# Kernel optimization log

Measured on AMD Instinct MI355X. Metric: run time of the kernel, lower is better.

Reference implementation:

```python
import jax, jax.numpy as jnp
import numpy as np

N = 100000      # nodes
E = 1600000     # edges (avg degree 16)
D_IN, D_H, D_OUT = 128, 128, 64
EPS = 1e-5      # BatchNorm1d eps


def setup_inputs() -> dict:
    key = jax.random.key(0)
    ks = jax.random.split(key, 8)
    x = jax.random.normal(ks[0], (N, D_IN), jnp.float32)
    edge_index = jax.random.randint(ks[1], (2, E), 0, N, dtype=jnp.int64)

    def glorot(k, i, o):
        return jax.random.normal(k, (i, o), jnp.float32) * np.float32(1.0 / np.sqrt(i))

    return {
        "x": x,
        "edge_index": edge_index,
        "W1": glorot(ks[2], D_IN, D_H), "b1": jnp.zeros((D_H,), jnp.float32),
        "g1": jnp.ones((D_H,), jnp.float32), "be1": jnp.zeros((D_H,), jnp.float32),
        "W2": glorot(ks[3], D_H, D_H), "b2": jnp.zeros((D_H,), jnp.float32),
        "g2": jnp.ones((D_H,), jnp.float32), "be2": jnp.zeros((D_H,), jnp.float32),
        "W3": glorot(ks[4], D_H, D_OUT), "b3": jnp.zeros((D_OUT,), jnp.float32),
    }


def gcn_conv(h, W, b, src, dst, norm_e, self_norm):
    # GCNConv: D^{-1/2}(A+I)D^{-1/2} h W + b  (self-loops handled analytically)
    hw = h @ W                                  # [N, out]
    msg = hw[src] * norm_e[:, None]             # [E, out] gather + scale
    agg = jax.ops.segment_sum(msg, dst, num_segments=N)
    return agg + hw * self_norm[:, None] + b


def batchnorm(x, g, b):
    mu = jnp.mean(x, axis=0)
    var = jnp.var(x, axis=0)
    return (x - mu) * jax.lax.rsqrt(var + EPS) * g + b


def reference(x, edge_index, W1, b1, g1, be1, W2, b2, g2, be2, W3, b3):
    src, dst = edge_index[0], edge_index[1]
    # degrees including self-loop
    deg = jax.ops.segment_sum(jnp.ones((E,), jnp.float32), dst, num_segments=N) + 1.0
    dis = jax.lax.rsqrt(deg)                    # deg^{-1/2}
    norm_e = dis[src] * dis[dst]                # per-edge norm
    self_norm = dis * dis                       # self-loop norm deg^{-1}

    h = jax.nn.relu(batchnorm(gcn_conv(x, W1, b1, src, dst, norm_e, self_norm), g1, be1))
    h = jax.nn.relu(batchnorm(gcn_conv(h, W2, b2, src, dst, norm_e, self_norm), g2, be2))
    return gcn_conv(h, W3, b3, src, dst, norm_e, self_norm)
```

## Files before the change

kernel.cpp:

```cpp
#include <hip/hip_runtime.h>
#include <hip/hip_bf16.h>

#define BN_EPS 1e-5f
#define BINSH 9
#define MAXNB 200
#define NBLK 256

typedef __attribute__((ext_vector_type(8))) short bf16x8v;
typedef __attribute__((ext_vector_type(4))) float f32x4v;

__device__ __forceinline__ float u2f(unsigned x) { return __uint_as_float(x); }
__device__ __forceinline__ unsigned short f2bf(float f) {
    union { __hip_bfloat16 h; unsigned short u; } cv;
    cv.h = __float2bfloat16(f);
    return cv.u;
}

__device__ __forceinline__ int edge_at(const void* p, long long i, int is64) {
    return is64 ? (int)((const long long*)p)[i] : ((const int*)p)[i];
}

__device__ __forceinline__ int detect_is64(const void* eidx, int* sflag, int t) {
    if (t == 0) {
        const int* e32 = (const int*)eidx;
        int nz = 0;
        for (int i = 0; i < 64; ++i) nz += (e32[2 * i + 1] != 0);
        *sflag = (nz == 0) ? 1 : 0;
    }
    return 0;
}

__global__ __launch_bounds__(256) void histA_kernel(const void* __restrict__ eidx,
                                                    int* __restrict__ hist2dT,
                                                    int* __restrict__ binhist,
                                                    int E, int NB, int per_block) {
    __shared__ int lh[MAXNB];
    __shared__ int sflag;
    const int t = threadIdx.x;
    detect_is64(eidx, &sflag, t);
    for (int i = t; i < NB; i += 256) lh[i] = 0;
    __syncthreads();
    const int is64 = sflag;
    long long base = (long long)blockIdx.x * per_block;
    long long lim  = base + per_block;
    if (lim > E) lim = E;
    for (long long e = base + t; e < lim; e += 256) {
        int d = edge_at(eidx, (long long)E + e, is64);
        atomicAdd(&lh[d >> BINSH], 1);
    }
    __syncthreads();
    for (int i = t; i < NB; i += 256) {
        hist2dT[i * NBLK + blockIdx.x] = lh[i];
        atomicAdd(&binhist[i], lh[i]);
    }
}

__global__ void binscan_kernel(const int* __restrict__ binhist, int* __restrict__ binrp, int NB) {
    __shared__ int s[256];
    const int t = threadIdx.x;
    int v = (t < NB) ? binhist[t] : 0;
    s[t] = v;
    __syncthreads();
    for (int off = 1; off < 256; off <<= 1) {
        int x = (t >= off) ? s[t - off] : 0;
        __syncthreads();
        s[t] += x;
        __syncthreads();
    }
    if (t < NB) binrp[t] = s[t] - v;
    if (t == 0) binrp[NB] = s[255];
}

__global__ __launch_bounds__(256) void colscan_kernel(int* __restrict__ hist2dT,
                                                      const int* __restrict__ binrp) {
    __shared__ int s[256];
    const int b = blockIdx.x;
    const int t = threadIdx.x;
    int v = hist2dT[b * NBLK + t];
    s[t] = v;
    __syncthreads();
    for (int off = 1; off < 256; off <<= 1) {
        int x = (t >= off) ? s[t - off] : 0;
        __syncthreads();
        s[t] += x;
        __syncthreads();
    }
    hist2dT[b * NBLK + t] = binrp[b] + s[t] - v;
}

__global__ __launch_bounds__(256) void passB_kernel(const void* __restrict__ eidx,
                                                    const int* __restrict__ hist2dT,
                                                    int2* __restrict__ ibuf,
                                                    int E, int NB, int per_block) {
    __shared__ int lbase[MAXNB];
    __shared__ int lcur[MAXNB];
    __shared__ int sflag;
    const int t = threadIdx.x;
    detect_is64(eidx, &sflag, t);
    for (int i = t; i < NB; i += 256) {
        lbase[i] = hist2dT[i * NBLK + blockIdx.x];
        lcur[i]  = 0;
    }
    __syncthreads();
    const int is64 = sflag;
    long long base = (long long)blockIdx.x * per_block;
    long long lim  = base + per_block;
    if (lim > E) lim = E;
    for (long long e = base + t; e < lim; e += 256) {
        int sN = edge_at(eidx, e, is64);
        int d  = edge_at(eidx, (long long)E + e, is64);
        int b  = d >> BINSH;
        int pos = lbase[b] + atomicAdd(&lcur[b], 1);
        ibuf[pos] = make_int2(sN, d);
    }
}

__global__ __launch_bounds__(256) void binsort2_kernel(const int2* __restrict__ ibuf,
                                                       const int* __restrict__ binrp,
                                                       int* __restrict__ rp,
                                                       float* __restrict__ dis,
                                                       int2* __restrict__ ep, int N) {
    const int b  = blockIdx.x;
    const int d0 = b << BINSH;
    const int dc = min(1 << BINSH, N - d0);
    __shared__ int lcnt[1 << BINSH];
    __shared__ int lofs[1 << BINSH];
    __shared__ int s2[256];
    const int t = threadIdx.x;
    lcnt[t] = 0; lcnt[t + 256] = 0;
    __syncthreads();
    const int ib0 = binrp[b], ib1 = binrp[b + 1];
    const int nE  = ib1 - ib0;
    for (int i = t; i < nE; i += 256) {
        int2 sd = ibuf[ib0 + i];
        atomicAdd(&lcnt[sd.y - d0], 1);
    }
    __syncthreads();
    const int c0 = lcnt[2 * t], c1 = lcnt[2 * t + 1];
    const int pair = c0 + c1;
    s2[t] = pair;
    __syncthreads();
    for (int off = 1; off < 256; off <<= 1) {
        int x = (t >= off) ? s2[t - off] : 0;
        __syncthreads();
        s2[t] += x;
        __syncthreads();
    }
    const int pexcl = s2[t] - pair;
    if (2 * t < dc) {
        rp[d0 + 2 * t + 1] = ib0 + pexcl + c0;
        dis[d0 + 2 * t]    = rsqrtf((float)c0 + 1.0f);
    }
    if (2 * t + 1 < dc) {
        rp[d0 + 2 * t + 2] = ib0 + pexcl + pair;
        dis[d0 + 2 * t + 1] = rsqrtf((float)c1 + 1.0f);
    }
    if (b == 0 && t == 0) rp[0] = 0;
    lofs[2 * t]     = pexcl;
    lofs[2 * t + 1] = pexcl + c0;
    __syncthreads();
    for (int i = t; i < nE; i += 256) {
        int2 sd = ibuf[ib0 + i];
        int dl  = sd.y - d0;
        int pos = ib0 + atomicAdd(&lofs[dl], 1);
        ep[pos] = sd;
    }
}

__global__ void weight_kernel(int2* __restrict__ ep, const float* __restrict__ dis, int E) {
    int e = blockIdx.x * 256 + threadIdx.x;
    if (e >= E) return;
    int2 sd = ep[e];
    float w = dis[sd.x] * dis[sd.y];
    ep[e] = make_int2(sd.x, __float_as_int(w));
}

__global__ void prep_wt_all_kernel(const float* __restrict__ W1, const float* __restrict__ W2,
                                   const float* __restrict__ W3,
                                   __hip_bfloat16* __restrict__ wt1,
                                   __hip_bfloat16* __restrict__ wt2,
                                   __hip_bfloat16* __restrict__ wt3) {
    int i = blockIdx.x * 256 + threadIdx.x;
    if (i < 16384) {
        int k = i >> 7, c = i & 127;
        wt1[c * 128 + k] = __float2bfloat16(W1[i]);
    } else if (i < 32768) {
        int j = i - 16384;
        int k = j >> 7, c = j & 127;
        wt2[c * 128 + k] = __float2bfloat16(W2[j]);
    } else if (i < 40960) {
        int j = i - 32768;
        int k = j >> 6, c = j & 63;
        wt3[c * 128 + k] = __float2bfloat16(W3[j]);
    }
}

__device__ __forceinline__ void load8(const float* p, float* f) {
    float4 v0 = ((const float4*)p)[0];
    float4 v1 = ((const float4*)p)[1];
    f[0] = v0.x; f[1] = v0.y; f[2] = v0.z; f[3] = v0.w;
    f[4] = v1.x; f[5] = v1.y; f[6] = v1.z; f[7] = v1.w;
}
__device__ __forceinline__ void load8(const __hip_bfloat16* p, float* f) {
    uint4 v = *(const uint4*)p;
    f[0] = u2f(v.x << 16); f[1] = u2f(v.x & 0xffff0000u);
    f[2] = u2f(v.y << 16); f[3] = u2f(v.y & 0xffff0000u);
    f[4] = u2f(v.z << 16); f[5] = u2f(v.z & 0xffff0000u);
    f[6] = u2f(v.w << 16); f[7] = u2f(v.w & 0xffff0000u);
}

template <int DOUT, bool BN, typename TH>
__global__ __launch_bounds__(256) void mfma_gemm_kernel(const TH* __restrict__ H,
                                                        const __hip_bfloat16* __restrict__ Wt,
                                                        const float* __restrict__ stats,
                                                        const float* __restrict__ g,
                                                        const float* __restrict__ be,
                                                        float invN,
                                                        __hip_bfloat16* __restrict__ out, int N) {
    constexpr int NCT = DOUT / 16;
    constexpr int LDW = 136;
    __shared__ __hip_bfloat16 sWt[DOUT * LDW];
    __shared__ float sBN[256];
    const int t = threadIdx.x;
    for (int i = t; i < DOUT * 16; i += 256) {
        int row = i >> 4, seg = i & 15;
        *(uint4*)&sWt[row * LDW + seg * 8] = ((const uint4*)Wt)[i];
    }
    if (BN && t < 128) {
        float mu  = stats[t] * invN;
        float var = stats[128 + t] * invN - mu * mu;
        float sc  = g[t] * rsqrtf(var + BN_EPS);
        sBN[t]       = sc;
        sBN[128 + t] = be[t] - mu * sc;
    }
    __syncthreads();
    const int lane = t & 63, wid = t >> 6;
    const int kq = lane >> 4, mrow = lane & 15;
    const int grow = blockIdx.x * 64 + wid * 16 + mrow;
    const int lrow = min(grow, N - 1);
    bf16x8v afrag[4];
#pragma unroll
    for (int ks = 0; ks < 4; ++ks) {
        const int k0 = ks * 32 + kq * 8;
        float f[8];
        load8(H + (size_t)lrow * 128 + k0, f);
        if (BN) {
            float4 s0 = *(const float4*)&sBN[k0];
            float4 s1 = *(const float4*)&sBN[k0 + 4];
            float4 h0 = *(const float4*)&sBN[128 + k0];
            float4 h1 = *(const float4*)&sBN[128 + k0 + 4];
            f[0] = fmaxf(fmaf(f[0], s0.x, h0.x), 0.f);
            f[1] = fmaxf(fmaf(f[1], s0.y, h0.y), 0.f);
            f[2] = fmaxf(fmaf(f[2], s0.z, h0.z), 0.f);
            f[3] = fmaxf(fmaf(f[3], s0.w, h0.w), 0.f);
            f[4] = fmaxf(fmaf(f[4], s1.x, h1.x), 0.f);
            f[5] = fmaxf(fmaf(f[5], s1.y, h1.y), 0.f);
            f[6] = fmaxf(fmaf(f[6], s1.z, h1.z), 0.f);
            f[7] = fmaxf(fmaf(f[7], s1.w, h1.w), 0.f);
        }
        bf16x8v a;
#pragma unroll
        for (int j = 0; j < 8; ++j) a[j] = (short)f2bf(f[j]);
        afrag[ks] = a;
    }
    f32x4v acc[NCT];
#pragma unroll
    for (int ct = 0; ct < NCT; ++ct) acc[ct] = (f32x4v){0.f, 0.f, 0.f, 0.f};
#pragma unroll
    for (int ct = 0; ct < NCT; ++ct) {
#pragma unroll
        for (int ks = 0; ks < 4; ++ks) {
            bf16x8v b = *(const bf16x8v*)&sWt[(ct * 16 + mrow) * LDW + ks * 32 + kq * 8];
            acc[ct] = __builtin_amdgcn_mfma_f32_16x16x32_bf16(afrag[ks], b, acc[ct], 0, 0, 0);
        }
    }
#pragma unroll
    for (int r = 0; r < 4; ++r) {
        int orow = blockIdx.x * 64 + wid * 16 + kq * 4 + r;
        if (orow < N) {
            __hip_bfloat16* op = out + (size_t)orow * DOUT + mrow;
#pragma unroll
            for (int ct = 0; ct < NCT; ++ct) {
                union { unsigned short u; __hip_bfloat16 h; } cv;
                cv.u = f2bf(acc[ct][r]);
                op[ct * 16] = cv.h;
            }
        }
    }
}

__device__ __forceinline__ void acc8(float* a, uint4 v, float w) {
    a[0] += u2f(v.x << 16) * w;  a[1] += u2f(v.x & 0xffff0000u) * w;
    a[2] += u2f(v.y << 16) * w;  a[3] += u2f(v.y & 0xffff0000u) * w;
    a[4] += u2f(v.z << 16) * w;  a[5] += u2f(v.z & 0xffff0000u) * w;
    a[6] += u2f(v.w << 16) * w;  a[7] += u2f(v.w & 0xffff0000u) * w;
}

template <int D, bool OUTBF>
__global__ __launch_bounds__(256) void agg_kernel(const __hip_bfloat16* __restrict__ hw,
                                                  const int* __restrict__ rp,
                                                  const int2* __restrict__ ep,
                                                  const float* __restrict__ dis,
                                                  const float* __restrict__ bias,
                                                  void* __restrict__ outv, int N) {
    constexpr int LPR = D / 8;
    const int t = threadIdx.x;
    const int gtid = blockIdx.x * 256 + t;
    const int n    = gtid / LPR;
    const int lane = gtid % LPR;
    if (n >= N) return;
    const uint4* hw8 = (const uint4*)hw;
    float a[8] = {0.f, 0.f, 0.f, 0.f, 0.f, 0.f, 0.f, 0.f};
    float sn = dis[n];
    sn *= sn;
    uint4 hv = hw8[(size_t)n * LPR + lane];
    acc8(a, hv, sn);
    int e0 = rp[n], e1 = rp[n + 1];
    int e = e0;
    for (; e + 8 <= e1; e += 8) {
        int2 p[8];
        uint4 v[8];
#pragma unroll
        for (int j = 0; j < 8; ++j) p[j] = ep[e + j];
#pragma unroll
        for (int j = 0; j < 8; ++j) v[j] = hw8[(size_t)p[j].x * LPR + lane];
#pragma unroll
        for (int j = 0; j < 8; ++j) acc8(a, v[j], __int_as_float(p[j].y));
    }
    for (; e + 4 <= e1; e += 4) {
        int2 p[4];
        uint4 v[4];
#pragma unroll
        for (int j = 0; j < 4; ++j) p[j] = ep[e + j];
#pragma unroll
        for (int j = 0; j < 4; ++j) v[j] = hw8[(size_t)p[j].x * LPR + lane];
#pragma unroll
        for (int j = 0; j < 4; ++j) acc8(a, v[j], __int_as_float(p[j].y));
    }
    for (; e < e1; ++e) {
        int2 p = ep[e];
        uint4 v = hw8[(size_t)p.x * LPR + lane];
        acc8(a, v, __int_as_float(p.y));
    }
    float4 b0 = *(const float4*)(bias + lane * 8);
    float4 b1 = *(const float4*)(bias + lane * 8 + 4);
    a[0] += b0.x; a[1] += b0.y; a[2] += b0.z; a[3] += b0.w;
    a[4] += b1.x; a[5] += b1.y; a[6] += b1.z; a[7] += b1.w;
    if (OUTBF) {
        uint4 o;
        o.x = (unsigned)f2bf(a[0]) | ((unsigned)f2bf(a[1]) << 16);
        o.y = (unsigned)f2bf(a[2]) | ((unsigned)f2bf(a[3]) << 16);
        o.z = (unsigned)f2bf(a[4]) | ((unsigned)f2bf(a[5]) << 16);
        o.w = (unsigned)f2bf(a[6]) | ((unsigned)f2bf(a[7]) << 16);
        ((uint4*)outv)[(size_t)n * LPR + lane] = o;
    } else {
        float4* op = (float4*)outv + ((size_t)n * D + lane * 8) / 4;
        op[0] = make_float4(a[0], a[1], a[2], a[3]);
        op[1] = make_float4(a[4], a[5], a[6], a[7]);
    }
}

__global__ void bn_stats_kernel(const __hip_bfloat16* __restrict__ X, float* __restrict__ stats, int N) {
    const int t  = threadIdx.x;
    const int c4 = t & 31;
    const int rg = t >> 5;
    const uint2* X4 = (const uint2*)X;
    float s0=0,s1=0,s2=0,s3=0,q0=0,q1=0,q2=0,q3=0;
    for (int r = blockIdx.x * 8 + rg; r < N; r += gridDim.x * 8) {
        uint2 v = X4[(size_t)r * 32 + c4];
        float f0 = u2f(v.x << 16), f1 = u2f(v.x & 0xffff0000u);
        float f2 = u2f(v.y << 16), f3 = u2f(v.y & 0xffff0000u);
        s0 += f0; q0 += f0 * f0;
        s1 += f1; q1 += f1 * f1;
        s2 += f2; q2 += f2 * f2;
        s3 += f3; q3 += f3 * f3;
    }
    __shared__ float ls[8][32][8];
    ls[rg][c4][0] = s0; ls[rg][c4][1] = s1; ls[rg][c4][2] = s2; ls[rg][c4][3] = s3;
    ls[rg][c4][4] = q0; ls[rg][c4][5] = q1; ls[rg][c4][6] = q2; ls[rg][c4][7] = q3;
    __syncthreads();
    if (t < 32) {
        float a[8] = {0,0,0,0,0,0,0,0};
        for (int g = 0; g < 8; ++g)
            for (int k = 0; k < 8; ++k) a[k] += ls[g][t][k];
        for (int k = 0; k < 4; ++k) {
            atomicAdd(&stats[t * 4 + k], a[k]);
            atomicAdd(&stats[128 + t * 4 + k], a[4 + k]);
        }
    }
}

extern "C" void kernel_launch(void* const* d_in, const int* in_sizes, int n_in,
                              void* d_out, int out_size, void* d_ws, size_t ws_size,
                              hipStream_t stream) {
    const float* x   = (const float*)d_in[0];
    const void*  eix = d_in[1];
    const float* W1  = (const float*)d_in[2];
    const float* b1  = (const float*)d_in[3];
    const float* g1  = (const float*)d_in[4];
    const float* be1 = (const float*)d_in[5];
    const float* W2  = (const float*)d_in[6];
    const float* b2  = (const float*)d_in[7];
    const float* g2  = (const float*)d_in[8];
    const float* be2 = (const float*)d_in[9];
    const float* W3  = (const float*)d_in[10];
    const float* b3  = (const float*)d_in[11];
    float* outp = (float*)d_out;

    const int N = in_sizes[0] / 128;
    const int E = in_sizes[1] / 2;
    const int NB = (N + (1 << BINSH) - 1) >> BINSH;

    char* base = (char*)d_ws;
    size_t off = 0;
    auto alloc = [&](size_t bytes) -> char* {
        char* p = base + off;
        off = (off + bytes + 255) & ~(size_t)255;
        return p;
    };
    __hip_bfloat16* A = (__hip_bfloat16*)alloc((size_t)N * 128 * 2);
    __hip_bfloat16* B = (__hip_bfloat16*)alloc((size_t)N * 128 * 2);
    int*   rp      = (int*)alloc((size_t)(N + 1) * 4);
    float* dis     = (float*)alloc((size_t)N * 4);
    int2*  ep      = (int2*)alloc((size_t)E * 8);
    int2*  ibuf    = (int2*)alloc((size_t)E * 8);
    int*   hist2dT = (int*)alloc((size_t)MAXNB * NBLK * 4);
    int*   binrp   = (int*)alloc((MAXNB + 1) * 4);
    int*   binhist = (int*)alloc(MAXNB * 4);
    float* stats1  = (float*)alloc(256 * 4);
    float* stats2  = (float*)alloc(256 * 4);
    __hip_bfloat16* wt1 = (__hip_bfloat16*)alloc(128 * 128 * 2);
    __hip_bfloat16* wt2 = (__hip_bfloat16*)alloc(128 * 128 * 2);
    __hip_bfloat16* wt3 = (__hip_bfloat16*)alloc(64 * 128 * 2);
    (void)ws_size; (void)n_in; (void)out_size;

    const int per_block = (E + NBLK - 1) / NBLK;

    hipMemsetAsync(binhist, 0, 3 * 1024, stream);
    histA_kernel<<<NBLK, 256, 0, stream>>>(eix, hist2dT, binhist, E, NB, per_block);
    binscan_kernel<<<1, 256, 0, stream>>>(binhist, binrp, NB);
    colscan_kernel<<<NB, 256, 0, stream>>>(hist2dT, binrp);
    passB_kernel<<<NBLK, 256, 0, stream>>>(eix, hist2dT, ibuf, E, NB, per_block);
    binsort2_kernel<<<NB, 256, 0, stream>>>(ibuf, binrp, rp, dis, ep, N);
    weight_kernel<<<(E + 255) / 256, 256, 0, stream>>>(ep, dis, E);
    prep_wt_all_kernel<<<160, 256, 0, stream>>>(W1, W2, W3, wt1, wt2, wt3);

    const float invN = 1.0f / (float)N;
    const int gemm_grid   = (N + 63) / 64;
    const int agg128_grid = (int)(((long long)N * 16 + 255) / 256);
    const int agg64_grid  = (int)(((long long)N * 8 + 255) / 256);

    mfma_gemm_kernel<128, false, float><<<gemm_grid, 256, 0, stream>>>(
        x, wt1, nullptr, nullptr, nullptr, 0.f, A, N);
    agg_kernel<128, true><<<agg128_grid, 256, 0, stream>>>(A, rp, ep, dis, b1, B, N);
    bn_stats_kernel<<<256, 256, 0, stream>>>(B, stats1, N);

    mfma_gemm_kernel<128, true, __hip_bfloat16><<<gemm_grid, 256, 0, stream>>>(
        B, wt2, stats1, g1, be1, invN, A, N);
    agg_kernel<128, true><<<agg128_grid, 256, 0, stream>>>(A, rp, ep, dis, b2, B, N);
    bn_stats_kernel<<<256, 256, 0, stream>>>(B, stats2, N);

    mfma_gemm_kernel<64, true, __hip_bfloat16><<<gemm_grid, 256, 0, stream>>>(
        B, wt3, stats2, g2, be2, invN, A, N);
    agg_kernel<64, false><<<agg64_grid, 256, 0, stream>>>(A, rp, ep, dis, b3, outp, N);
}
```

Before: 369.7 us.

## Sort nodes by degree for aggregation and drop per-edge weight array

Removes the weight_kernel and stores only source indices in the CSR edge array, computing the normalization as dis[src] inside the aggregation and factoring dis[dst] out as one final multiply. Adds a counting sort of nodes by in-degree (capped at 63) that produces a permutation, so neighbouring threads in a wavefront handle nodes with similar degree and diverge less. This halves edge-array traffic and removes one pass over the edges, at the cost of an extra scattered dis[] gather per edge, a non-contiguous output order, four small extra kernels, and a shorter 4-wide unroll instead of 8-wide.

```diff
diff --git a/kernel.cpp b/kernel.cpp
--- a/kernel.cpp
+++ b/kernel.cpp
@@ -119,7 +119,7 @@
                                                        const int* __restrict__ binrp,
                                                        int* __restrict__ rp,
                                                        float* __restrict__ dis,
-                                                       int2* __restrict__ ep, int N) {
+                                                       int* __restrict__ ep, int N) {
     const int b  = blockIdx.x;
     const int d0 = b << BINSH;
     const int dc = min(1 << BINSH, N - d0);
@@ -163,16 +163,73 @@
         int2 sd = ibuf[ib0 + i];
         int dl  = sd.y - d0;
         int pos = ib0 + atomicAdd(&lofs[dl], 1);
-        ep[pos] = sd;
-    }
-}
-
-__global__ void weight_kernel(int2* __restrict__ ep, const float* __restrict__ dis, int E) {
-    int e = blockIdx.x * 256 + threadIdx.x;
-    if (e >= E) return;
-    int2 sd = ep[e];
-    float w = dis[sd.x] * dis[sd.y];
-    ep[e] = make_int2(sd.x, __float_as_int(w));
+        ep[pos] = sd.x;
+    }
+}
+
+__global__ __launch_bounds__(256) void degA_kernel(const int* __restrict__ rp, int* __restrict__ dblk,
+                                                   int* __restrict__ gdeg, int N, int NDB) {
+    __shared__ int lh[64];
+    const int t = threadIdx.x;
+    if (t < 64) lh[t] = 0;
+    __syncthreads();
+    int n = blockIdx.x * 256 + t;
+    if (n < N) {
+        int deg = min(rp[n + 1] - rp[n], 63);
+        atomicAdd(&lh[deg], 1);
+    }
+    __syncthreads();
+    if (t < 64) {
+        dblk[t * NDB + blockIdx.x] = lh[t];
+        atomicAdd(&gdeg[t], lh[t]);
+    }
+}
+
+__global__ void degscan_kernel(const int* __restrict__ gdeg, int* __restrict__ degbase) {
+    __shared__ int s[64];
+    const int t = threadIdx.x;
+    int v = gdeg[t];
+    s[t] = v;
+    __syncthreads();
+    for (int off = 1; off < 64; off <<= 1) {
+        int x = (t >= off) ? s[t - off] : 0;
+        __syncthreads();
+        s[t] += x;
+        __syncthreads();
+    }
+    degbase[t] = s[t] - v;
+}
+
+__global__ __launch_bounds__(512) void degcol_kernel(int* __restrict__ dblk,
+                                                     const int* __restrict__ degbase, int NDB) {
+    __shared__ int s[512];
+    const int d = blockIdx.x;
+    const int t = threadIdx.x;
+    int v = (t < NDB) ? dblk[d * NDB + t] : 0;
+    s[t] = v;
+    __syncthreads();
+    for (int off = 1; off < 512; off <<= 1) {
+        int x = (t >= off) ? s[t - off] : 0;
+        __syncthreads();
+        s[t] += x;
+        __syncthreads();
+    }
+    if (t < NDB) dblk[d * NDB + t] = degbase[d] + s[t] - v;
+}
+
+__global__ __launch_bounds__(256) void degscat_kernel(const int* __restrict__ rp,
+                                                      const int* __restrict__ dblk,
+                                                      int* __restrict__ perm, int N, int NDB) {
+    __shared__ int lcur[64];
+    const int t = threadIdx.x;
+    if (t < 64) lcur[t] = 0;
+    __syncthreads();
+    int n = blockIdx.x * 256 + t;
+    if (n < N) {
+        int deg = min(rp[n + 1] - rp[n], 63);
+        int slot = atomicAdd(&lcur[deg], 1);
+        perm[dblk[deg * NDB + blockIdx.x] + slot] = n;
+    }
 }
 
 __global__ void prep_wt_all_kernel(const float* __restrict__ W1, const float* __restrict__ W2,
@@ -299,53 +356,50 @@
 template <int D, bool OUTBF>
 __global__ __launch_bounds__(256) void agg_kernel(const __hip_bfloat16* __restrict__ hw,
                                                   const int* __restrict__ rp,
-                                                  const int2* __restrict__ ep,
+                                                  const int* __restrict__ ep,
                                                   const float* __restrict__ dis,
+                                                  const int* __restrict__ perm,
                                                   const float* __restrict__ bias,
                                                   void* __restrict__ outv, int N) {
     constexpr int LPR = D / 8;
     const int t = threadIdx.x;
     const int gtid = blockIdx.x * 256 + t;
-    const int n    = gtid / LPR;
+    const int idx  = gtid / LPR;
     const int lane = gtid % LPR;
-    if (n >= N) return;
+    if (idx >= N) return;
+    const int n = perm[idx];
     const uint4* hw8 = (const uint4*)hw;
     float a[8] = {0.f, 0.f, 0.f, 0.f, 0.f, 0.f, 0.f, 0.f};
-    float sn = dis[n];
-    sn *= sn;
+    const float dn = dis[n];
     uint4 hv = hw8[(size_t)n * LPR + lane];
-    acc8(a, hv, sn);
+    acc8(a, hv, dn);
     int e0 = rp[n], e1 = rp[n + 1];
     int e = e0;
-    for (; e + 8 <= e1; e += 8) {
-        int2 p[8];
-        uint4 v[8];
-#pragma unroll
-        for (int j = 0; j < 8; ++j) p[j] = ep[e + j];
-#pragma unroll
-        for (int j = 0; j < 8; ++j) v[j] = hw8[(size_t)p[j].x * LPR + lane];
-#pragma unroll
-        for (int j = 0; j < 8; ++j) acc8(a, v[j], __int_as_float(p[j].y));
-    }
     for (; e + 4 <= e1; e += 4) {
-        int2 p[4];
-        uint4 v[4];
-#pragma unroll
-        for (int j = 0; j < 4; ++j) p[j] = ep[e + j];
-#pragma unroll
-        for (int j = 0; j < 4; ++j) v[j] = hw8[(size_t)p[j].x * LPR + lane];
-#pragma unroll
-        for (int j = 0; j < 4; ++j) acc8(a, v[j], __int_as_float(p[j].y));
+        int p0 = ep[e + 0];
+        int p1 = ep[e + 1];
+        int p2 = ep[e + 2];
+        int p3 = ep[e + 3];
+        uint4 v0 = hw8[(size_t)p0 * LPR + lane];
+        uint4 v1 = hw8[(size_t)p1 * LPR + lane];
+        uint4 v2 = hw8[(size_t)p2 * LPR + lane];
+        uint4 v3 = hw8[(size_t)p3 * LPR + lane];
+        acc8(a, v0, dis[p0]);
+        acc8(a, v1, dis[p1]);
+        acc8(a, v2, dis[p2]);
+        acc8(a, v3, dis[p3]);
     }
     for (; e < e1; ++e) {
-        int2 p = ep[e];
-        uint4 v = hw8[(size_t)p.x * LPR + lane];
-        acc8(a, v, __int_as_float(p.y));
+        int p = ep[e];
+        uint4 v = hw8[(size_t)p * LPR + lane];
+        acc8(a, v, dis[p]);
     }
     float4 b0 = *(const float4*)(bias + lane * 8);
     float4 b1 = *(const float4*)(bias + lane * 8 + 4);
-    a[0] += b0.x; a[1] += b0.y; a[2] += b0.z; a[3] += b0.w;
-    a[4] += b1.x; a[5] += b1.y; a[6] += b1.z; a[7] += b1.w;
+    a[0] = fmaf(a[0], dn, b0.x); a[1] = fmaf(a[1], dn, b0.y);
+    a[2] = fmaf(a[2], dn, b0.z); a[3] = fmaf(a[3], dn, b0.w);
+    a[4] = fmaf(a[4], dn, b1.x); a[5] = fmaf(a[5], dn, b1.y);
+    a[6] = fmaf(a[6], dn, b1.z); a[7] = fmaf(a[7], dn, b1.w);
     if (OUTBF) {
         uint4 o;
         o.x = (unsigned)f2bf(a[0]) | ((unsigned)f2bf(a[1]) << 16);
@@ -410,6 +464,7 @@
     const int N = in_sizes[0] / 128;
     const int E = in_sizes[1] / 2;
     const int NB = (N + (1 << BINSH) - 1) >> BINSH;
+    const int NDB = (N + 255) / 256;
 
     char* base = (char*)d_ws;
     size_t off = 0;
@@ -422,13 +477,17 @@
     __hip_bfloat16* B = (__hip_bfloat16*)alloc((size_t)N * 128 * 2);
     int*   rp      = (int*)alloc((size_t)(N + 1) * 4);
     float* dis     = (float*)alloc((size_t)N * 4);
-    int2*  ep      = (int2*)alloc((size_t)E * 8);
+    int*   ep      = (int*)alloc((size_t)E * 4);
     int2*  ibuf    = (int2*)alloc((size_t)E * 8);
     int*   hist2dT = (int*)alloc((size_t)MAXNB * NBLK * 4);
     int*   binrp   = (int*)alloc((MAXNB + 1) * 4);
+    int*   perm    = (int*)alloc((size_t)N * 4);
+    int*   dblk    = (int*)alloc((size_t)64 * NDB * 4);
+    int*   degbase = (int*)alloc(64 * 4);
     int*   binhist = (int*)alloc(MAXNB * 4);
     float* stats1  = (float*)alloc(256 * 4);
     float* stats2  = (float*)alloc(256 * 4);
+    int*   gdeg    = (int*)alloc(64 * 4);
     __hip_bfloat16* wt1 = (__hip_bfloat16*)alloc(128 * 128 * 2);
     __hip_bfloat16* wt2 = (__hip_bfloat16*)alloc(128 * 128 * 2);
     __hip_bfloat16* wt3 = (__hip_bfloat16*)alloc(64 * 128 * 2);
@@ -436,13 +495,16 @@
 
     const int per_block = (E + NBLK - 1) / NBLK;
 
-    hipMemsetAsync(binhist, 0, 3 * 1024, stream);
+    hipMemsetAsync(binhist, 0, 3 * 1024 + 256, stream);
     histA_kernel<<<NBLK, 256, 0, stream>>>(eix, hist2dT, binhist, E, NB, per_block);
     binscan_kernel<<<1, 256, 0, stream>>>(binhist, binrp, NB);
     colscan_kernel<<<NB, 256, 0, stream>>>(hist2dT, binrp);
     passB_kernel<<<NBLK, 256, 0, stream>>>(eix, hist2dT, ibuf, E, NB, per_block);
     binsort2_kernel<<<NB, 256, 0, stream>>>(ibuf, binrp, rp, dis, ep, N);
-    weight_kernel<<<(E + 255) / 256, 256, 0, stream>>>(ep, dis, E);
+    degA_kernel<<<NDB, 256, 0, stream>>>(rp, dblk, gdeg, N, NDB);
+    degscan_kernel<<<1, 64, 0, stream>>>(gdeg, degbase);
+    degcol_kernel<<<64, 512, 0, stream>>>(dblk, degbase, NDB);
+    degscat_kernel<<<NDB, 256, 0, stream>>>(rp, dblk, perm, N, NDB);
     prep_wt_all_kernel<<<160, 256, 0, stream>>>(W1, W2, W3, wt1, wt2, wt3);
 
     const float invN = 1.0f / (float)N;
@@ -452,15 +514,15 @@
 
     mfma_gemm_kernel<128, false, float><<<gemm_grid, 256, 0, stream>>>(
         x, wt1, nullptr, nullptr, nullptr, 0.f, A, N);
-    agg_kernel<128, true><<<agg128_grid, 256, 0, stream>>>(A, rp, ep, dis, b1, B, N);
+    agg_kernel<128, true><<<agg128_grid, 256, 0, stream>>>(A, rp, ep, dis, perm, b1, B, N);
     bn_stats_kernel<<<256, 256, 0, stream>>>(B, stats1, N);
 
     mfma_gemm_kernel<128, true, __hip_bfloat16><<<gemm_grid, 256, 0, stream>>>(
         B, wt2, stats1, g1, be1, invN, A, N);
-    agg_kernel<128, true><<<agg128_grid, 256, 0, stream>>>(A, rp, ep, dis, b2, B, N);
+    agg_kernel<128, true><<<agg128_grid, 256, 0, stream>>>(A, rp, ep, dis, perm, b2, B, N);
     bn_stats_kernel<<<256, 256, 0, stream>>>(B, stats2, N);
 
     mfma_gemm_kernel<64, true, __hip_bfloat16><<<gemm_grid, 256, 0, stream>>>(
         B, wt3, stats2, g2, be2, invN, A, N);
-    agg_kernel<64, false><<<agg64_grid, 256, 0, stream>>>(A, rp, ep, dis, b3, outp, N);
-}
+    agg_kernel<64, false><<<agg64_grid, 256, 0, stream>>>(A, rp, ep, dis, perm, b3, outp, N);
+}
```

After: 371.8 us. About the same (+0.6%).
